# Kernel optimization log

Hardware: AMD Instinct MI355X
Metric: run time of the kernel (lower is better)

## Reference

```python
import math
import jax, jax.numpy as jnp
import numpy as np

KSIZE = (5, 5)
SIGMA = (1.0, 1.0)
LOW_T = 0.1
HIGH_T = 0.2
EPS = 1e-6

# Sobel first-order kernels (cross-correlation form, unnormalized as in canny)
SOBEL = np.array([[[-1., 0., 1.], [-2., 0., 2.], [-1., 0., 1.]],
                  [[-1., -2., -1.], [0., 0., 0.], [1., 2., 1.]]], np.float32)

# Neighbor offsets in kornia's direction order: 0deg=right, going clockwise
_OFFS = [(1, 2), (2, 2), (2, 1), (2, 0), (1, 0), (0, 0), (0, 1), (0, 2)]

def _nms_kernels():
    k = np.zeros((8, 1, 3, 3), np.float32)
    k[:, 0, 1, 1] = 1.0
    for i, (r, c) in enumerate(_OFFS):
        k[i, 0, r, c] = -1.0
    return jnp.asarray(k)

def _hysteresis_kernels():
    k = np.zeros((8, 1, 3, 3), np.float32)
    for i, (r, c) in enumerate(_OFFS):
        k[i, 0, r, c] = 1.0
    return jnp.asarray(k)

def _gaussian_kernel1d(ksize, sigma):
    x = jnp.arange(ksize, dtype=jnp.float32) - ksize // 2
    if ksize % 2 == 0:
        x = x + 0.5
    g = jnp.exp(-x * x / (2.0 * sigma * sigma))
    return g / g.sum()

def _conv_depthwise_same(x, k2d, pad_mode):
    # x: [B, C, H, W]; k2d: [kh, kw]; cross-correlation with 'same' output
    b, c, h, w = x.shape
    kh, kw = k2d.shape
    xp = jnp.pad(x, ((0, 0), (0, 0),
                     ((kh - 1) // 2, kh - 1 - (kh - 1) // 2),
                     ((kw - 1) // 2, kw - 1 - (kw - 1) // 2)), mode=pad_mode)
    xr = xp.reshape(b * c, 1, h + kh - 1, w + kw - 1)
    out = jax.lax.conv_general_dilated(xr, k2d[None, None].astype(x.dtype), (1, 1), 'VALID')
    return out.reshape(b, c, h, w)

def _conv_multi(x, w, p):
    # x: [B, 1, H, W], w: [O, 1, kh, kw], zero padding p
    return jax.lax.conv_general_dilated(x, w.astype(x.dtype), (1, 1), [(p, p), (p, p)])

def canny_fwd(x):
    dtype = x.dtype
    if x.shape[1] == 3:  # rgb -> grayscale
        wgt = jnp.array([0.299, 0.587, 0.114], dtype)
        x = jnp.einsum('bchw,c->bhw', x, wgt)[:, None]
    # Gaussian blur, separable, reflect padding
    kx = _gaussian_kernel1d(KSIZE[1], SIGMA[1])
    ky = _gaussian_kernel1d(KSIZE[0], SIGMA[0])
    blurred = _conv_depthwise_same(x, kx[None, :], 'reflect')
    blurred = _conv_depthwise_same(blurred, ky[:, None], 'reflect')
    # Sobel gradients, replicate padding, unnormalized
    gx = _conv_depthwise_same(blurred, jnp.asarray(SOBEL[0]), 'edge')
    gy = _conv_depthwise_same(blurred, jnp.asarray(SOBEL[1]), 'edge')
    magnitude = jnp.sqrt(gx * gx + gy * gy + EPS)  # [B,1,H,W]
    # quantized gradient direction index in {0..7}
    ang = jnp.round(jnp.arctan2(gy, gx) * (180.0 / math.pi) / 45.0)
    # direction-aware non-maximum suppression
    nms_mag = _conv_multi(magnitude, _nms_kernels(), 1)  # [B,8,H,W]
    pos = jnp.mod(ang, 8.0).astype(jnp.int32)
    neg = jnp.mod(ang + 4.0, 8.0).astype(jnp.int32)
    sel_p = jnp.take_along_axis(nms_mag, pos, axis=1)
    sel_n = jnp.take_along_axis(nms_mag, neg, axis=1)
    is_max = jnp.minimum(sel_p, sel_n) > 0.0
    magnitude = magnitude * is_max
    # double threshold: weak=0.5, strong=1.0
    low = (magnitude > LOW_T).astype(dtype)
    high = (magnitude > HIGH_T).astype(dtype)
    edges = (low + high) * 0.5
    # hysteresis: grow strong into weak until fixed point (flood fill)
    hk = _hysteresis_kernels()
    edges0 = jax.lax.stop_gradient(edges)

    def body(carry):
        e, _ = carry
        weak = (e == 0.5).astype(dtype)
        strong = (e == 1.0).astype(dtype)
        nb = _conv_multi(e, hk, 1)  # 8 neighbor values
        mag = jnp.any(nb == 1.0, axis=1, keepdims=True).astype(dtype)
        mag = mag * weak + strong
        return mag + (mag == 0.0) * weak * 0.5, e

    def cond(carry):
        e, e_old = carry
        return jnp.any(e != e_old)

    e_final, _ = jax.lax.while_loop(cond, body, (edges0, -jnp.ones_like(edges0)))
    # at the fixed point the returned hysteresis magnitude is exactly (edges == 1)
    edges_out = (e_final == 1.0).astype(dtype)
    return magnitude, edges_out

def setup_inputs() -> dict:
    key = jax.random.key(0)
    x = jax.random.uniform(key, (4, 3, 1024, 1024), dtype=jnp.float32)
    return {'x': x}

def reference(x):
    return canny_fwd(x)
```

## Files before the change

### kernel.cpp

```cpp
#include <hip/hip_runtime.h>
#include <math.h>

static constexpr int BB  = 4;
static constexpr int HH  = 1024;
static constexpr int WW  = 1024;
static constexpr int HWP = HH * WW;
static constexpr int NPIX = BB * HWP;
static constexpr int WPR = WW / 64;
static constexpr int PW  = HWP / 64;
static constexpr int ROUNDS = 10;
static constexpr int NT  = BB * 8 * 8;
static constexpr int RF  = ROUNDS + 1;
static constexpr int FCN = RF + RF * NT;

static constexpr int TX = 64, TY = 16;
static constexpr int GH = 24,  GW = 72;
static constexpr int HBH = 24, HBW = 68;
static constexpr int VBH = 20, VBW = 68;
static constexpr int MGH = 18, MGW = 66;

__device__ __forceinline__ int reflect_idx(int i, int n) {
    i = (i < 0) ? -i : i;
    return (i >= n) ? (2 * n - 2 - i) : i;
}

__global__ void __launch_bounds__(256) k_front(const float* __restrict__ x,
                                               float* __restrict__ out0,
                                               unsigned long long* __restrict__ weakP,
                                               unsigned long long* __restrict__ strongP,
                                               int* __restrict__ fc,
                                               double w0, double w1, double w2) {
    __shared__ double A[GH * GW];
    __shared__ double B[HBH * HBW];
    __shared__ unsigned char P[TY * TX];

    const int tid = threadIdx.x;
    const int x0  = blockIdx.x * TX;
    const int y0  = blockIdx.y * TY;
    const int b   = blockIdx.z;
    const float* base = x + (size_t)b * 3u * HWP;

    if (blockIdx.x == 0 && blockIdx.y == 0 && b == 0) {
        for (int i = tid; i < FCN; i += 256)
            fc[i] = (i == 0 || (i >= RF && i < RF + NT)) ? 1 : 0;
    }

    for (int idx = tid; idx < GH * GW; idx += 256) {
        int r = idx / GW, c = idx - r * GW;
        int gyr = reflect_idx(y0 + r - 4, HH);
        int gxr = reflect_idx(x0 + c - 4, WW);
        const float* rp = base + (size_t)gyr * WW;
        double rr = (double)rp[gxr];
        double gg = (double)rp[HWP + gxr];
        double bb = (double)rp[2 * HWP + gxr];
        A[idx] = rr * 0.299 + gg * 0.587 + bb * 0.114;
    }
    __syncthreads();

    for (int idx = tid; idx < HBH * HBW; idx += 256) {
        int r = idx / HBW, c = idx - r * HBW;
        const double* g = &A[r * GW + c];
        double s;
        s  = w0 * g[0];
        s += w1 * g[1];
        s += w2 * g[2];
        s += w1 * g[3];
        s += w0 * g[4];
        B[idx] = s;
    }
    __syncthreads();

    for (int idx = tid; idx < VBH * VBW; idx += 256) {
        int r = idx / VBW, c = idx - r * VBW;
        const double* h = &B[r * HBW + c];
        double s;
        s  = w0 * h[0];
        s += w1 * h[1 * HBW];
        s += w2 * h[2 * HBW];
        s += w1 * h[3 * HBW];
        s += w0 * h[4 * HBW];
        A[idx] = s;
    }
    __syncthreads();

    for (int idx = tid; idx < MGH * MGW; idx += 256) {
        int r = idx / MGW, c = idx - r * MGW;
        int gy = y0 + r - 1, gx = x0 + c - 1;
        double mg2 = 0.0;
        if (gy >= 0 && gy < HH && gx >= 0 && gx < WW) {
            int ym = gy > 0 ? gy - 1 : 0, yp = gy < HH - 1 ? gy + 1 : HH - 1;
            int xm = gx > 0 ? gx - 1 : 0, xp = gx < WW - 1 ? gx + 1 : WW - 1;
            auto BL = [&](int yy, int xx) -> double {
                return A[(yy - y0 + 2) * VBW + (xx - x0 + 2)];
            };
            double b00 = BL(ym, xm), b01 = BL(ym, gx), b02 = BL(ym, xp);
            double b10 = BL(gy, xm),                   b12 = BL(gy, xp);
            double b20 = BL(yp, xm), b21 = BL(yp, gx), b22 = BL(yp, xp);
            double gxv = -b00 + b02 - 2.0 * b10 + 2.0 * b12 - b20 + b22;
            double gyv = -b00 - 2.0 * b01 - b02 + b20 + 2.0 * b21 + b22;
            mg2 = gxv * gxv + gyv * gyv + 1e-6;
            if (r >= 1 && r < TY + 1 && c >= 1 && c < TX + 1) {
                double ax = fabs(gxv), ay = fabs(gyv);
                int p;
                if (ay < 0.41421356237309503 * ax)
                    p = (gxv >= 0.0) ? 0 : 4;
                else if (ay < 2.4142135623730951 * ax)
                    p = (gyv >= 0.0) ? ((gxv >= 0.0) ? 1 : 3)
                                     : ((gxv >= 0.0) ? 7 : 5);
                else
                    p = (gyv >= 0.0) ? 2 : 6;
                P[(r - 1) * TX + (c - 1)] = (unsigned char)p;
            }
        }
        B[r * MGW + c] = mg2;
    }
    __syncthreads();

    for (int k = 0; k < (TX * TY) / 256; ++k) {
        int idx = k * 256 + tid;
        int r = idx >> 6, c = idx & 63;
        double ctr2 = B[(r + 1) * MGW + (c + 1)];
        int p = P[idx];
        int dr = ((425   >> (2 * p)) & 3) - 1;
        int dc = ((36890 >> (2 * p)) & 3) - 1;
        double mp2 = B[(r + 1 + dr) * MGW + (c + 1 + dc)];
        double mn2 = B[(r + 1 - dr) * MGW + (c + 1 - dc)];
        bool ismax = (ctr2 > mp2) && (ctr2 > mn2);
        out0[(size_t)b * HWP + (size_t)(y0 + r) * WW + (x0 + c)] =
            ismax ? (float)sqrt(ctr2) : 0.0f;
        bool strong = ismax && (ctr2 > 0.04);
        bool weak   = ismax && (ctr2 > 0.01) && !strong;
        unsigned long long wb = __ballot(weak);
        unsigned long long sb = __ballot(strong);
        if ((tid & 63) == 0) {
            int word = (y0 + r) * WPR + (x0 >> 6);
            weakP[(size_t)b * PW + word]   = wb;
            strongP[(size_t)b * PW + word] = sb;
        }
    }
}

__device__ __forceinline__ unsigned long long ks_fill(unsigned long long g, unsigned long long p) {
    unsigned long long q;
    q = p;        g |= q & (g << 1);
    q &= q << 1;  g |= q & (g << 2);
    q &= q << 2;  g |= q & (g << 4);
    q &= q << 4;  g |= q & (g << 8);
    q &= q << 8;  g |= q & (g << 16);
    q &= q << 16; g |= q & (g << 32);
    q = p;        g |= q & (g >> 1);
    q &= q >> 1;  g |= q & (g >> 2);
    q &= q >> 2;  g |= q & (g >> 4);
    q &= q >> 4;  g |= q & (g >> 8);
    q &= q >> 8;  g |= q & (g >> 16);
    q &= q >> 16; g |= q & (g >> 32);
    return g;
}

__global__ void __launch_bounds__(256) k_pass(const unsigned long long* __restrict__ weakP,
                                              unsigned long long* __restrict__ strongP,
                                              int* __restrict__ flags,
                                              int* __restrict__ dirt,
                                              float* __restrict__ out1, int rr) {
    __shared__ unsigned long long S[128][2];
    __shared__ int chf[4];

    const int tid  = threadIdx.x;
    const int lane = tid & 63;
    const int w    = tid >> 6;
    const int wy   = w >> 1, wx = w & 1;
    const int tile = blockIdx.x;
    const int b  = tile >> 6;
    const int ty = (tile >> 3) & 7;
    const int tx = tile & 7;
    const int tb = b << 6;

    unsigned long long* spl = strongP + (size_t)b * PW;
    const int row  = (ty << 7) + (wy << 6) + lane;
    const int wc   = (tx << 1) + wx;
    const int wi   = row * WPR + wc;
    const int lrow = (wy << 6) + lane;

    const bool active = (flags[rr - 1] != 0);
    if (!active && rr != ROUNDS) return;

    int go = 0;
    if (active) {
        const int* d0 = dirt + (size_t)(rr - 1) * NT;
        if (ty > 0) { go |= d0[tb + ((ty - 1) << 3) + tx];
                      if (tx > 0) go |= d0[tb + ((ty - 1) << 3) + tx - 1];
                      if (tx < 7) go |= d0[tb + ((ty - 1) << 3) + tx + 1]; }
        if (ty < 7) { go |= d0[tb + ((ty + 1) << 3) + tx];
                      if (tx > 0) go |= d0[tb + ((ty + 1) << 3) + tx - 1];
                      if (tx < 7) go |= d0[tb + ((ty + 1) << 3) + tx + 1]; }
        if (tx > 0) go |= d0[tb + (ty << 3) + tx - 1];
        if (tx < 7) go |= d0[tb + (ty << 3) + tx + 1];
    }

    if (go) {
        const unsigned long long* wp = weakP + (size_t)b * PW;
        unsigned long long wv = wp[wi];
        unsigned long long s  = spl[wi];

        unsigned long long ho_ext = 0;
        if (wx == 0) { if (tx > 0) ho_ext = spl[wi - 1] >> 63; }
        else         { if (tx < 7) ho_ext = spl[wi + 1] << 63; }
        unsigned long long topE = 0, botE = 0;
        unsigned long long topC = 0, botC = 0;
        if (lane == 0) {
            if (wy == 0) {
                if (ty > 0) {
                    int ra = row - 1;
                    unsigned long long hs = spl[ra * WPR + wc];
                    topE = (hs << 1) | hs | (hs >> 1);
                    if (wc > 0)  topE |= spl[ra * WPR + wc - 1] >> 63;
                    if (wc < 15) topE |= spl[ra * WPR + wc + 1] << 63;
                }
            } else {
                int rb = row - 1;
                if (wx == 0) { if (tx > 0) topC = spl[rb * WPR + wc - 1] >> 63; }
                else         { if (tx < 7) topC = spl[rb * WPR + wc + 1] << 63; }
            }
        }
        if (lane == 63) {
            if (wy == 1) {
                if (ty < 7) {
                    int ra = row + 1;
                    unsigned long long hs = spl[ra * WPR + wc];
                    botE = (hs << 1) | hs | (hs >> 1);
                    if (wc > 0)  botE |= spl[ra * WPR + wc - 1] >> 63;
                    if (wc < 15) botE |= spl[ra * WPR + wc + 1] << 63;
                }
            } else {
                int rb = row + 1;
                if (wx == 0) { if (tx > 0) botC = spl[rb * WPR + wc - 1] >> 63; }
                else         { if (tx < 7) botC = spl[rb * WPR + wc + 1] << 63; }
            }
        }

        S[lrow][wx] = s;
        if (lane == 0) chf[w] = 0;
        __syncthreads();

        unsigned long long pub = s;
        int blkchanged = 0;
        for (;;) {
            unsigned long long partner = S[lrow][wx ^ 1];
            unsigned long long ho = ho_ext | ((wx == 1) ? (partner >> 63) : (partner << 63));
            unsigned long long top = 0, bot = 0;
            if (lane == 0) {
                if (wy == 1) {
                    unsigned long long a = S[63][wx], p2 = S[63][wx ^ 1];
                    top = (a << 1) | a | (a >> 1) |
                          ((wx == 1) ? (p2 >> 63) : (p2 << 63)) | topC;
                } else top = topE;
            }
            if (lane == 63) {
                if (wy == 0) {
                    unsigned long long a = S[64][wx], p2 = S[64][wx ^ 1];
                    bot = (a << 1) | a | (a >> 1) |
                          ((wx == 1) ? (p2 >> 63) : (p2 << 63)) | botC;
                } else bot = botE;
            }

            for (;;) {
                unsigned long long sp = (s << 1) | s | (s >> 1) | ho;
                unsigned long long up = __shfl_up(sp, 1);
                unsigned long long dn = __shfl_down(sp, 1);
                if (lane == 0)  up = top;
                if (lane == 63) dn = bot;
                unsigned long long g = s | (wv & (up | sp | dn));
                g = ks_fill(g, wv);
                int ch = (g != s);
                s = g;
                if (!__any(ch)) break;
            }

            int wch = __any(s != pub);
            if (lane == 0) chf[w] = wch;
            __syncthreads();
            S[lrow][wx] = s;
            pub = s;
            int any = chf[0] | chf[1] | chf[2] | chf[3];
            if (any) blkchanged = 1;
            __syncthreads();
            if (!any) break;
        }

        if (blkchanged) {
            spl[wi] = s;
            if (tid == 0) {
                dirt[(size_t)rr * NT + tb + (ty << 3) + tx] = 1;
                atomicOr(&flags[rr], 1);
            }
        }
    }

    if (rr == ROUNDS) {
        if (!go) S[lrow][wx] = spl[wi];
        __syncthreads();
        float* o = out1 + (size_t)b * HWP;
        for (int it = 0; it < 16; ++it) {
            int fi = (it << 8) + tid;
            int r  = fi >> 5;
            int c4 = fi & 31;
            unsigned long long bits = S[r][c4 >> 4];
            int sh = (c4 & 15) << 2;
            float4 v;
            v.x = ((bits >> (sh + 0)) & 1ull) ? 1.0f : 0.0f;
            v.y = ((bits >> (sh + 1)) & 1ull) ? 1.0f : 0.0f;
            v.z = ((bits >> (sh + 2)) & 1ull) ? 1.0f : 0.0f;
            v.w = ((bits >> (sh + 3)) & 1ull) ? 1.0f : 0.0f;
            int grow = (ty << 7) + r;
            int gcol = (tx << 7) + (c4 << 2);
            *reinterpret_cast<float4*>(&o[(size_t)grow * WW + gcol]) = v;
        }
    }
}

extern "C" void kernel_launch(void* const* d_in, const int* in_sizes, int n_in,
                              void* d_out, int out_size, void* d_ws, size_t ws_size,
                              hipStream_t stream) {
    const float* x = (const float*)d_in[0];
    float* out0 = (float*)d_out;
    float* out1 = out0 + NPIX;

    unsigned long long* weakP   = (unsigned long long*)d_ws;
    unsigned long long* strongP = weakP + (size_t)BB * PW;
    int* fc    = (int*)(strongP + (size_t)BB * PW);
    int* flags = fc;
    int* dirt  = fc + RF;

    double g0 = exp(-2.0), g1 = exp(-0.5), g2 = 1.0;
    double sum = (((g0 + g1) + g2) + g1) + g0;
    double w0 = g0 / sum, w1 = g1 / sum, w2 = g2 / sum;

    k_front<<<dim3(WW / TX, HH / TY, BB), dim3(256), 0, stream>>>(
        x, out0, weakP, strongP, fc, w0, w1, w2);

    for (int r = 1; r <= ROUNDS; ++r)
        k_pass<<<dim3(NT), dim3(256), 0, stream>>>(weakP, strongP, flags, dirt, out1, r);
}
```

Measured before the change: 153.0 us.

## Fuse hysteresis rounds into one cooperative kernel with neighbor-tile counters

Replaces the ten separate hysteresis-pass launches with a single cooperative kernel that loops over the rounds internally. Each tile waits only on its eight neighbor tiles' progress counters, using acquire loads and release stores, instead of a full grid barrier. This removes per-round launch overhead and the global flag, and keeps the tile state in registers across rounds. In exchange it relies on all 256 blocks being co-resident and on careful memory ordering through relaxed atomics plus fences.

```diff
diff --git a/kernel.cpp b/kernel.cpp
--- a/kernel.cpp
+++ b/kernel.cpp
@@ -11,13 +11,18 @@
 static constexpr int ROUNDS = 10;
 static constexpr int NT  = BB * 8 * 8;
 static constexpr int RF  = ROUNDS + 1;
-static constexpr int FCN = RF + RF * NT;
+static constexpr int FCN = NT + RF * NT;
 
 static constexpr int TX = 64, TY = 16;
 static constexpr int GH = 24,  GW = 72;
 static constexpr int HBH = 24, HBW = 68;
 static constexpr int VBH = 20, VBW = 68;
 static constexpr int MGH = 18, MGW = 66;
+
+#define AL_U64(p)  __hip_atomic_load((p), __ATOMIC_RELAXED, __HIP_MEMORY_SCOPE_AGENT)
+#define AS_U64(p,v) __hip_atomic_store((p), (v), __ATOMIC_RELAXED, __HIP_MEMORY_SCOPE_AGENT)
+#define AL_I(p)    __hip_atomic_load((p), __ATOMIC_RELAXED, __HIP_MEMORY_SCOPE_AGENT)
+#define AS_I(p,v)  __hip_atomic_store((p), (v), __ATOMIC_RELAXED, __HIP_MEMORY_SCOPE_AGENT)
 
 __device__ __forceinline__ int reflect_idx(int i, int n) {
     i = (i < 0) ? -i : i;
@@ -42,7 +47,7 @@
 
     if (blockIdx.x == 0 && blockIdx.y == 0 && b == 0) {
         for (int i = tid; i < FCN; i += 256)
-            fc[i] = (i == 0 || (i >= RF && i < RF + NT)) ? 1 : 0;
+            fc[i] = (i >= NT && i < 2 * NT) ? 1 : 0;
     }
 
     for (int idx = tid; idx < GH * GW; idx += 256) {
@@ -157,13 +162,14 @@
     return g;
 }
 
-__global__ void __launch_bounds__(256) k_pass(const unsigned long long* __restrict__ weakP,
+__global__ void __launch_bounds__(256) k_hyst(const unsigned long long* __restrict__ weakP,
                                               unsigned long long* __restrict__ strongP,
-                                              int* __restrict__ flags,
+                                              int* __restrict__ cnt,
                                               int* __restrict__ dirt,
-                                              float* __restrict__ out1, int rr) {
+                                              float* __restrict__ out1) {
     __shared__ unsigned long long S[128][2];
     __shared__ int chf[4];
+    __shared__ int goS;
 
     const int tid  = threadIdx.x;
     const int lane = tid & 63;
@@ -175,146 +181,164 @@
     const int tx = tile & 7;
     const int tb = b << 6;
 
-    unsigned long long* spl = strongP + (size_t)b * PW;
+    unsigned long long* spl      = strongP + (size_t)b * PW;
+    const unsigned long long* wp = weakP + (size_t)b * PW;
     const int row  = (ty << 7) + (wy << 6) + lane;
     const int wc   = (tx << 1) + wx;
     const int wi   = row * WPR + wc;
     const int lrow = (wy << 6) + lane;
 
-    const bool active = (flags[rr - 1] != 0);
-    if (!active && rr != ROUNDS) return;
-
-    int go = 0;
-    if (active) {
-        const int* d0 = dirt + (size_t)(rr - 1) * NT;
-        if (ty > 0) { go |= d0[tb + ((ty - 1) << 3) + tx];
-                      if (tx > 0) go |= d0[tb + ((ty - 1) << 3) + tx - 1];
-                      if (tx < 7) go |= d0[tb + ((ty - 1) << 3) + tx + 1]; }
-        if (ty < 7) { go |= d0[tb + ((ty + 1) << 3) + tx];
-                      if (tx > 0) go |= d0[tb + ((ty + 1) << 3) + tx - 1];
-                      if (tx < 7) go |= d0[tb + ((ty + 1) << 3) + tx + 1]; }
-        if (tx > 0) go |= d0[tb + (ty << 3) + tx - 1];
-        if (tx < 7) go |= d0[tb + (ty << 3) + tx + 1];
-    }
-
-    if (go) {
-        const unsigned long long* wp = weakP + (size_t)b * PW;
-        unsigned long long wv = wp[wi];
-        unsigned long long s  = spl[wi];
-
-        unsigned long long ho_ext = 0;
-        if (wx == 0) { if (tx > 0) ho_ext = spl[wi - 1] >> 63; }
-        else         { if (tx < 7) ho_ext = spl[wi + 1] << 63; }
-        unsigned long long topE = 0, botE = 0;
-        unsigned long long topC = 0, botC = 0;
-        if (lane == 0) {
-            if (wy == 0) {
-                if (ty > 0) {
-                    int ra = row - 1;
-                    unsigned long long hs = spl[ra * WPR + wc];
-                    topE = (hs << 1) | hs | (hs >> 1);
-                    if (wc > 0)  topE |= spl[ra * WPR + wc - 1] >> 63;
-                    if (wc < 15) topE |= spl[ra * WPR + wc + 1] << 63;
-                }
-            } else {
-                int rb = row - 1;
-                if (wx == 0) { if (tx > 0) topC = spl[rb * WPR + wc - 1] >> 63; }
-                else         { if (tx < 7) topC = spl[rb * WPR + wc + 1] << 63; }
-            }
-        }
-        if (lane == 63) {
-            if (wy == 1) {
-                if (ty < 7) {
-                    int ra = row + 1;
-                    unsigned long long hs = spl[ra * WPR + wc];
-                    botE = (hs << 1) | hs | (hs >> 1);
-                    if (wc > 0)  botE |= spl[ra * WPR + wc - 1] >> 63;
-                    if (wc < 15) botE |= spl[ra * WPR + wc + 1] << 63;
-                }
-            } else {
-                int rb = row + 1;
-                if (wx == 0) { if (tx > 0) botC = spl[rb * WPR + wc - 1] >> 63; }
-                else         { if (tx < 7) botC = spl[rb * WPR + wc + 1] << 63; }
-            }
-        }
-
-        S[lrow][wx] = s;
-        if (lane == 0) chf[w] = 0;
+    int nbr = -1;
+    if (tid < 8) {
+        const int dys[8] = {-1,-1,-1, 0, 0, 1, 1, 1};
+        const int dxs[8] = {-1, 0, 1,-1, 1,-1, 0, 1};
+        int yy = ty + dys[tid], xx = tx + dxs[tid];
+        if (yy >= 0 && yy < 8 && xx >= 0 && xx < 8) nbr = tb + (yy << 3) + xx;
+    }
+
+    unsigned long long wv = wp[wi];
+    unsigned long long s  = spl[wi];
+
+    for (int rr = 1; rr <= ROUNDS; ++rr) {
+        if (rr > 1 && tid < 8 && nbr >= 0) {
+            while (__hip_atomic_load(&cnt[nbr], __ATOMIC_ACQUIRE,
+                                     __HIP_MEMORY_SCOPE_AGENT) < rr - 1)
+                __builtin_amdgcn_s_sleep(1);
+        }
         __syncthreads();
 
-        unsigned long long pub = s;
-        int blkchanged = 0;
-        for (;;) {
-            unsigned long long partner = S[lrow][wx ^ 1];
-            unsigned long long ho = ho_ext | ((wx == 1) ? (partner >> 63) : (partner << 63));
-            unsigned long long top = 0, bot = 0;
+        if (tid == 0) {
+            const int* d0 = dirt + (size_t)(rr - 1) * NT;
+            int go = 0;
+            if (ty > 0) { go |= AL_I(&d0[tb + ((ty - 1) << 3) + tx]);
+                          if (tx > 0) go |= AL_I(&d0[tb + ((ty - 1) << 3) + tx - 1]);
+                          if (tx < 7) go |= AL_I(&d0[tb + ((ty - 1) << 3) + tx + 1]); }
+            if (ty < 7) { go |= AL_I(&d0[tb + ((ty + 1) << 3) + tx]);
+                          if (tx > 0) go |= AL_I(&d0[tb + ((ty + 1) << 3) + tx - 1]);
+                          if (tx < 7) go |= AL_I(&d0[tb + ((ty + 1) << 3) + tx + 1]); }
+            if (tx > 0) go |= AL_I(&d0[tb + (ty << 3) + tx - 1]);
+            if (tx < 7) go |= AL_I(&d0[tb + (ty << 3) + tx + 1]);
+            goS = go;
+        }
+        __syncthreads();
+
+        if (goS) {
+            unsigned long long ho_ext = 0;
+            if (wx == 0) { if (tx > 0) ho_ext = AL_U64(&spl[wi - 1]) >> 63; }
+            else         { if (tx < 7) ho_ext = AL_U64(&spl[wi + 1]) << 63; }
+            unsigned long long topE = 0, botE = 0;
+            unsigned long long topC = 0, botC = 0;
             if (lane == 0) {
+                if (wy == 0) {
+                    if (ty > 0) {
+                        int ra = row - 1;
+                        unsigned long long hs = AL_U64(&spl[ra * WPR + wc]);
+                        topE = (hs << 1) | hs | (hs >> 1);
+                        if (wc > 0)  topE |= AL_U64(&spl[ra * WPR + wc - 1]) >> 63;
+                        if (wc < 15) topE |= AL_U64(&spl[ra * WPR + wc + 1]) << 63;
+                    }
+                } else {
+                    int rb = row - 1;
+                    if (wx == 0) { if (tx > 0) topC = AL_U64(&spl[rb * WPR + wc - 1]) >> 63; }
+                    else         { if (tx < 7) topC = AL_U64(&spl[rb * WPR + wc + 1]) << 63; }
+                }
+            }
+            if (lane == 63) {
                 if (wy == 1) {
-                    unsigned long long a = S[63][wx], p2 = S[63][wx ^ 1];
-                    top = (a << 1) | a | (a >> 1) |
-                          ((wx == 1) ? (p2 >> 63) : (p2 << 63)) | topC;
-                } else top = topE;
-            }
-            if (lane == 63) {
-                if (wy == 0) {
-                    unsigned long long a = S[64][wx], p2 = S[64][wx ^ 1];
-                    bot = (a << 1) | a | (a >> 1) |
-                          ((wx == 1) ? (p2 >> 63) : (p2 << 63)) | botC;
-                } else bot = botE;
-            }
-
+                    if (ty < 7) {
+                        int ra = row + 1;
+                        unsigned long long hs = AL_U64(&spl[ra * WPR + wc]);
+                        botE = (hs << 1) | hs | (hs >> 1);
+                        if (wc > 0)  botE |= AL_U64(&spl[ra * WPR + wc - 1]) >> 63;
+                        if (wc < 15) botE |= AL_U64(&spl[ra * WPR + wc + 1]) << 63;
+                    }
+                } else {
+                    int rb = row + 1;
+                    if (wx == 0) { if (tx > 0) botC = AL_U64(&spl[rb * WPR + wc - 1]) >> 63; }
+                    else         { if (tx < 7) botC = AL_U64(&spl[rb * WPR + wc + 1]) << 63; }
+                }
+            }
+
+            S[lrow][wx] = s;
+            if (lane == 0) chf[w] = 0;
+            __syncthreads();
+
+            unsigned long long pub = s;
+            int blkchanged = 0;
             for (;;) {
-                unsigned long long sp = (s << 1) | s | (s >> 1) | ho;
-                unsigned long long up = __shfl_up(sp, 1);
-                unsigned long long dn = __shfl_down(sp, 1);
-                if (lane == 0)  up = top;
-                if (lane == 63) dn = bot;
-                unsigned long long g = s | (wv & (up | sp | dn));
-                g = ks_fill(g, wv);
-                int ch = (g != s);
-                s = g;
-                if (!__any(ch)) break;
-            }
-
-            int wch = __any(s != pub);
-            if (lane == 0) chf[w] = wch;
-            __syncthreads();
-            S[lrow][wx] = s;
-            pub = s;
-            int any = chf[0] | chf[1] | chf[2] | chf[3];
-            if (any) blkchanged = 1;
-            __syncthreads();
-            if (!any) break;
-        }
-
-        if (blkchanged) {
-            spl[wi] = s;
-            if (tid == 0) {
-                dirt[(size_t)rr * NT + tb + (ty << 3) + tx] = 1;
-                atomicOr(&flags[rr], 1);
-            }
-        }
-    }
-
-    if (rr == ROUNDS) {
-        if (!go) S[lrow][wx] = spl[wi];
+                unsigned long long partner = S[lrow][wx ^ 1];
+                unsigned long long ho = ho_ext | ((wx == 1) ? (partner >> 63) : (partner << 63));
+                unsigned long long top = 0, bot = 0;
+                if (lane == 0) {
+                    if (wy == 1) {
+                        unsigned long long a = S[63][wx], p2 = S[63][wx ^ 1];
+                        top = (a << 1) | a | (a >> 1) |
+                              ((wx == 1) ? (p2 >> 63) : (p2 << 63)) | topC;
+                    } else top = topE;
+                }
+                if (lane == 63) {
+                    if (wy == 0) {
+                        unsigned long long a = S[64][wx], p2 = S[64][wx ^ 1];
+                        bot = (a << 1) | a | (a >> 1) |
+                              ((wx == 1) ? (p2 >> 63) : (p2 << 63)) | botC;
+                    } else bot = botE;
+                }
+
+                for (;;) {
+                    unsigned long long sp = (s << 1) | s | (s >> 1) | ho;
+                    unsigned long long up = __shfl_up(sp, 1);
+                    unsigned long long dn = __shfl_down(sp, 1);
+                    if (lane == 0)  up = top;
+                    if (lane == 63) dn = bot;
+                    unsigned long long g = s | (wv & (up | sp | dn));
+                    g = ks_fill(g, wv);
+                    int ch = (g != s);
+                    s = g;
+                    if (!__any(ch)) break;
+                }
+
+                int wch = __any(s != pub);
+                if (lane == 0) chf[w] = wch;
+                __syncthreads();
+                S[lrow][wx] = s;
+                pub = s;
+                int any = chf[0] | chf[1] | chf[2] | chf[3];
+                if (any) blkchanged = 1;
+                __syncthreads();
+                if (!any) break;
+            }
+
+            if (blkchanged) {
+                AS_U64(&spl[wi], s);
+                if (tid == 0)
+                    AS_I(&dirt[(size_t)rr * NT + tile], 1);
+            }
+        }
+
         __syncthreads();
-        float* o = out1 + (size_t)b * HWP;
-        for (int it = 0; it < 16; ++it) {
-            int fi = (it << 8) + tid;
-            int r  = fi >> 5;
-            int c4 = fi & 31;
-            unsigned long long bits = S[r][c4 >> 4];
-            int sh = (c4 & 15) << 2;
-            float4 v;
-            v.x = ((bits >> (sh + 0)) & 1ull) ? 1.0f : 0.0f;
-            v.y = ((bits >> (sh + 1)) & 1ull) ? 1.0f : 0.0f;
-            v.z = ((bits >> (sh + 2)) & 1ull) ? 1.0f : 0.0f;
-            v.w = ((bits >> (sh + 3)) & 1ull) ? 1.0f : 0.0f;
-            int grow = (ty << 7) + r;
-            int gcol = (tx << 7) + (c4 << 2);
-            *reinterpret_cast<float4*>(&o[(size_t)grow * WW + gcol]) = v;
-        }
+        if (tid == 0) {
+            __threadfence();
+            __hip_atomic_store(&cnt[tile], rr, __ATOMIC_RELEASE, __HIP_MEMORY_SCOPE_AGENT);
+        }
+    }
+
+    S[lrow][wx] = s;
+    __syncthreads();
+    float* o = out1 + (size_t)b * HWP;
+    for (int it = 0; it < 16; ++it) {
+        int fi = (it << 8) + tid;
+        int r  = fi >> 5;
+        int c4 = fi & 31;
+        unsigned long long bits = S[r][c4 >> 4];
+        int sh = (c4 & 15) << 2;
+        float4 v;
+        v.x = ((bits >> (sh + 0)) & 1ull) ? 1.0f : 0.0f;
+        v.y = ((bits >> (sh + 1)) & 1ull) ? 1.0f : 0.0f;
+        v.z = ((bits >> (sh + 2)) & 1ull) ? 1.0f : 0.0f;
+        v.w = ((bits >> (sh + 3)) & 1ull) ? 1.0f : 0.0f;
+        int grow = (ty << 7) + r;
+        int gcol = (tx << 7) + (c4 << 2);
+        *reinterpret_cast<float4*>(&o[(size_t)grow * WW + gcol]) = v;
     }
 }
 
@@ -327,9 +351,9 @@
 
     unsigned long long* weakP   = (unsigned long long*)d_ws;
     unsigned long long* strongP = weakP + (size_t)BB * PW;
-    int* fc    = (int*)(strongP + (size_t)BB * PW);
-    int* flags = fc;
-    int* dirt  = fc + RF;
+    int* fc   = (int*)(strongP + (size_t)BB * PW);
+    int* cnt  = fc;
+    int* dirt = fc + NT;
 
     double g0 = exp(-2.0), g1 = exp(-0.5), g2 = 1.0;
     double sum = (((g0 + g1) + g2) + g1) + g0;
@@ -338,6 +362,6 @@
     k_front<<<dim3(WW / TX, HH / TY, BB), dim3(256), 0, stream>>>(
         x, out0, weakP, strongP, fc, w0, w1, w2);
 
-    for (int r = 1; r <= ROUNDS; ++r)
-        k_pass<<<dim3(NT), dim3(256), 0, stream>>>(weakP, strongP, flags, dirt, out1, r);
-}
+    void* args[] = {(void*)&weakP, (void*)&strongP, (void*)&cnt, (void*)&dirt, (void*)&out1};
+    hipLaunchCooperativeKernel((const void*)k_hyst, dim3(NT), dim3(256), args, 0, stream);
+}
```

After: 263.8 us. 72.4% more time.
